# Performance work log

Measured on AMD Instinct MI355X. Metric: run time of the kernel, lower is better.

Reference implementation:

```python
import jax, jax.numpy as jnp
import numpy as np
from jax import lax

# ---- constants mirroring Prediction.__init__ kwargs ----
INP = 608
NUM_CLASSES = 20
ALPHA, BETA = 1.0, 0.5
OBJ_T, CONF_T, LOC_T = 0.6, 0.05, 0.5
NMS_T, SIZE_T, SIGMA = 0.1, 0.0, 0.5
TOP_K = 8
M_CAND = 256          # fixed-size candidate cap for jit-compatible NMS
NEG = -1e9            # sentinel for masked scores
ANCHORS = [[(116, 90), (156, 198), (373, 326)],
           [(30, 61), (62, 45), (59, 119)],
           [(10, 13), (16, 30), (33, 23)]]


def _decode(pred, anchors):
    """pred: (B, A, G, G, 6+C) raw level output -> decoded flat tensors."""
    B, A, G, _, C = pred.shape
    stride = INP // G
    xy = jax.nn.sigmoid(pred[..., 0:2])
    g = jnp.arange(G, dtype=pred.dtype)
    gx, gy = jnp.meshgrid(g, g)                      # gx[i,j]=j, gy[i,j]=i (np.meshgrid 'xy')
    off = jnp.stack([gx, gy], axis=-1)[None, None]   # (1,1,G,G,2)
    xy = ALPHA * xy - 0.5 * (ALPHA - 1.0) + off
    anc = jnp.asarray(anchors, dtype=pred.dtype) / stride  # (A,2) scaled to grid units
    wh = jnp.exp(pred[..., 2:4]) * anc[None, :, None, None, :]
    box = jnp.concatenate([xy, wh], axis=-1) * stride       # back to pixel units
    obj = jax.nn.sigmoid(pred[..., 4])
    loc = jax.nn.sigmoid(pred[..., 5])
    clsp = jax.nn.softmax(pred[..., 6:], axis=-1)
    N = A * G * G
    return (box.reshape(B, N, 4), obj.reshape(B, N),
            loc.reshape(B, N), clsp.reshape(B, N, NUM_CLASSES))


def _soft_nms(boxes, s0, cls):
    """Per-image Gaussian soft-NMS (class-aware), +1 pixel IoU convention as in bbox_iou.
    boxes: (M,4) xyxy, s0: (M,) scores (NEG for invalid), cls: (M,) int. Returns kept mask."""
    M = s0.shape[0]

    def step(carry, _):
        s, kept = carry
        j = jnp.argmax(s)
        do = s[j] >= NMS_T
        kept = kept | ((jnp.arange(M) == j) & do)
        bj = boxes[j]
        ix1 = jnp.maximum(bj[0], boxes[:, 0]); iy1 = jnp.maximum(bj[1], boxes[:, 1])
        ix2 = jnp.minimum(bj[2], boxes[:, 2]); iy2 = jnp.minimum(bj[3], boxes[:, 3])
        inter = jnp.maximum(ix2 - ix1 + 1.0, 0.0) * jnp.maximum(iy2 - iy1 + 1.0, 0.0)
        a1 = (bj[2] - bj[0] + 1.0) * (bj[3] - bj[1] + 1.0)
        a2 = (boxes[:, 2] - boxes[:, 0] + 1.0) * (boxes[:, 3] - boxes[:, 1] + 1.0)
        iou = inter / (a1 + a2 - inter + 1e-16)
        decay = jnp.exp(-(iou * iou) / SIGMA)
        s_new = jnp.where(cls == cls[j], s * decay, s).at[j].set(NEG)
        s = jnp.where(do, s_new, s)
        return (s, kept), None

    (_, kept), _ = lax.scan(step, (s0, jnp.zeros(M, dtype=bool)), None, length=M)
    return kept


def _forward(pred_l0, pred_l1, pred_l2):
    parts = [_decode(p, a) for p, a in zip([pred_l0, pred_l1, pred_l2], ANCHORS)]
    box = jnp.concatenate([p[0] for p in parts], axis=1)   # (B,N,4) xywh
    obj = jnp.concatenate([p[1] for p in parts], axis=1)
    loc = jnp.concatenate([p[2] for p in parts], axis=1)
    clsp = jnp.concatenate([p[3] for p in parts], axis=1)

    cx, cy, w, h = box[..., 0], box[..., 1], box[..., 2], box[..., 3]
    x1 = jnp.clip(cx - w / 2, 0.0, INP); y1 = jnp.clip(cy - h / 2, 0.0, INP)
    x2 = jnp.clip(cx + w / 2, 0.0, INP); y2 = jnp.clip(cy + h / 2, 0.0, INP)
    boxes = jnp.stack([x1, y1, x2, y2], axis=-1)            # (B,N,4) xyxy, clamped

    cls_conf = jnp.max(clsp, axis=-1)
    cls_id = jnp.argmax(clsp, axis=-1)
    area = (x2 - x1) * (y2 - y1)
    valid = ((obj >= OBJ_T) & (area >= INP * INP * SIZE_T)
             & (obj * cls_conf >= CONF_T) & (loc >= LOC_T))
    score = (obj * cls_conf) ** BETA * loc ** (1.0 - BETA)
    masked = jnp.where(valid, score, NEG)

    # fixed-size candidate set per image (descending-score sort + cap)
    vals, idx = lax.top_k(masked, M_CAND)                   # (B,M)
    cboxes = jnp.take_along_axis(boxes, idx[..., None], axis=1)
    ccls = jnp.take_along_axis(cls_id, idx, axis=1)
    s0 = jnp.where(vals > NEG / 2, vals, NEG)

    kept = jax.vmap(_soft_nms)(cboxes, s0, ccls)            # (B,M) bool

    # keep_top_k: top_k among kept, ranked by ORIGINAL (pre-decay) score
    fscore = jnp.where(kept, vals, NEG)
    fvals, fidx = lax.top_k(fscore, TOP_K)                  # (B,TOP_K)
    fboxes = jnp.take_along_axis(cboxes, fidx[..., None], axis=1)
    fcls = jnp.take_along_axis(ccls, fidx, axis=1)
    row = jnp.concatenate([fboxes, fvals[..., None],
                           fcls[..., None].astype(fboxes.dtype)], axis=-1)  # (B,K,6)
    ok = fvals > NEG / 2
    return jnp.where(ok[..., None], row, 0.0)


def setup_inputs() -> dict:
    key = jax.random.key(0)
    k0, k1, k2 = jax.random.split(key, 3)
    return {
        "pred_l0": jax.random.normal(k0, (64, 3, 19, 19, 26), dtype=jnp.float32),
        "pred_l1": jax.random.normal(k1, (64, 3, 38, 38, 26), dtype=jnp.float32),
        "pred_l2": jax.random.normal(k2, (64, 3, 76, 76, 26), dtype=jnp.float32),
    }


def reference(pred_l0, pred_l1, pred_l2):
    return _forward(pred_l0, pred_l1, pred_l2)
```

## Files before the change

kernel.cpp:

```cpp
#include <hip/hip_runtime.h>
#include <climits>

constexpr int kB  = 64;
constexpr int kG0 = 19, kG1 = 38, kG2 = 76;
constexpr int kN0 = 3 * kG0 * kG0;
constexpr int kN1 = 3 * kG1 * kG1;
constexpr int kN2 = 3 * kG2 * kG2;
constexpr int kN  = kN0 + kN1 + kN2;
constexpr int kM  = 256;
constexpr int kTopK = 8;
constexpr float kNEG = -1e9f;

constexpr int kT0 = 5, kT1 = 17, kT2 = 68;
constexpr int kTilesPerImg = kT0 + kT1 + kT2;
constexpr int kGridScore = 1920;
constexpr int kTilesPerBlk = 3;

__constant__ float c_anchors[3][3][2] = {
    {{116.f, 90.f}, {156.f, 198.f}, {373.f, 326.f}},
    {{30.f, 61.f},  {62.f, 45.f},   {59.f, 119.f}},
    {{10.f, 13.f},  {16.f, 30.f},   {33.f, 23.f}},
};

__device__ __forceinline__ float fexpf(float x) { return __expf(x); }
__device__ __forceinline__ float frcpf(float x) { return __builtin_amdgcn_rcpf(x); }
__device__ __forceinline__ float fsigm(float x) { return frcpf(1.0f + __expf(-x)); }

__device__ __forceinline__ unsigned score_to_key(float s) {
  unsigned fb = __float_as_uint(s);
  unsigned m = (fb & 0x80000000u) ? 0xFFFFFFFFu : 0x80000000u;
  return fb ^ m;
}
__device__ __forceinline__ float key_to_score(unsigned k) {
  unsigned fb = (k & 0x80000000u) ? (k ^ 0x80000000u) : ~k;
  return __uint_as_float(fb);
}

__device__ __forceinline__ const float* cell_ptr(
    const float* p0, const float* p1, const float* p2, int b, int n,
    int& lvl, int& a, int& gi, int& gj, float& stride) {
  const float* src; int G, m;
  if (n < kN0)            { src = p0; G = kG0; lvl = 0; m = n;             stride = 32.f; }
  else if (n < kN0 + kN1) { src = p1; G = kG1; lvl = 1; m = n - kN0;       stride = 16.f; }
  else                    { src = p2; G = kG2; lvl = 2; m = n - kN0 - kN1; stride = 8.f; }
  int gg = G * G;
  a = m / gg;
  int r = m - a * gg;
  gi = r / G;
  gj = r - gi * G;
  return src + (size_t)((((b * 3 + a) * G + gi) * G + gj)) * 26;
}

__device__ __forceinline__ void waveArgmax(float& v, int& i) {
  #pragma unroll
  for (int off = 1; off < 64; off <<= 1) {
    float ov = __shfl_xor(v, off);
    int oi = __shfl_xor(i, off);
    if (ov > v || (ov == v && oi < i)) { v = ov; i = oi; }
  }
}
__device__ __forceinline__ float waveMax(float v) {
  #pragma unroll
  for (int off = 1; off < 64; off <<= 1) v = fmaxf(v, __shfl_xor(v, off));
  return v;
}
__device__ __forceinline__ float sel4f(const float a[4], int q) {
  float r = a[0];
  r = (q == 1) ? a[1] : r;
  r = (q == 2) ? a[2] : r;
  r = (q == 3) ? a[3] : r;
  return r;
}
__device__ __forceinline__ int sel4i(const int a[4], int q) {
  int r = a[0];
  r = (q == 1) ? a[1] : r;
  r = (q == 2) ? a[2] : r;
  r = (q == 3) ? a[3] : r;
  return r;
}

__device__ __forceinline__ void async_copy16(const void* g, void* s) {
  __builtin_amdgcn_global_load_lds(
      (__attribute__((address_space(1))) unsigned int*)g,
      (__attribute__((address_space(3))) unsigned int*)s, 16, 0, 0);
}

__global__ void zero_kernel(int* __restrict__ cnt) {
  if ((int)threadIdx.x < kB) cnt[threadIdx.x] = 0;
}

__global__ __launch_bounds__(256) void score_kernel(
    const float* __restrict__ p0, const float* __restrict__ p1, const float* __restrict__ p2,
    unsigned long long* __restrict__ pairs, int* __restrict__ cnt)
{
  __shared__ float2 lds2[2][256 * 13];
  __shared__ int wTot[4];
  __shared__ int sBase;

  int t = threadIdx.x;
  int lane = t & 63, wave = t >> 6;

  const float* gb[kTilesPerBlk]; int nc[kTilesPerBlk], n0[kTilesPerBlk], bb[kTilesPerBlk];
  bool dmaOk[kTilesPerBlk];
  #pragma unroll
  for (int j = 0; j < kTilesPerBlk; ++j) {
    int tileId = (int)blockIdx.x + j * kGridScore;
    int b = tileId / kTilesPerImg;
    int r = tileId - b * kTilesPerImg;
    const float* slab; int NL, lvlOff, tile; bool lvl0 = false;
    if (r < kT0)            { slab = p0; NL = kN0; lvlOff = 0;         tile = r;            lvl0 = true; }
    else if (r < kT0 + kT1) { slab = p1; NL = kN1; lvlOff = kN0;       tile = r - kT0; }
    else                    { slab = p2; NL = kN2; lvlOff = kN0 + kN1; tile = r - kT0 - kT1; }
    int cellBase = tile * 256;
    nc[j] = min(256, NL - cellBase);
    gb[j] = slab + ((size_t)b * NL + cellBase) * 26;
    n0[j] = lvlOff + cellBase;
    bb[j] = b;
    dmaOk[j] = (!lvl0) && (nc[j] == 256);
  }

  auto stage = [&](int j, int buf) {
    if (dmaOk[j]) {
      const char* g = (const char*)gb[j];
      char* s = (char*)&lds2[buf][0];
      for (int c = wave; c < 26; c += 4)
        async_copy16(g + c * 1024 + lane * 16, s + c * 1024);
    } else {
      const float2* g2 = (const float2*)gb[j];
      float2* s2 = &lds2[buf][0];
      int tot = nc[j] * 13;
      for (int i = t; i < tot; i += 256) s2[i] = g2[i];
    }
  };

  stage(0, 0);
  #pragma unroll
  for (int j = 0; j < kTilesPerBlk; ++j) {
    __syncthreads();
    if (j + 1 < kTilesPerBlk) stage(j + 1, (j + 1) & 1);

    int curNc = nc[j], curN0 = n0[j], curB = bb[j];
    const float2* bufp = &lds2[j & 1][0];

    bool valid = false;
    unsigned long long pairVal = 0;
    if (t < curNc) {
      const float2* c2 = &bufp[t * 13];
      float2 ol = c2[2];
      float obj = fsigm(ol.x);
      float loc = fsigm(ol.y);
      float tch[20];
      #pragma unroll
      for (int q = 0; q < 10; ++q) { float2 v = c2[3 + q]; tch[2*q] = v.x; tch[2*q+1] = v.y; }
      float lm = tch[0];
      #pragma unroll
      for (int c = 1; c < 20; ++c) lm = fmaxf(lm, tch[c]);
      float se = 0.f;
      #pragma unroll
      for (int c = 0; c < 20; ++c) se += fexpf(tch[c] - lm);
      float cls_conf = frcpf(se);
      float conf = obj * cls_conf;
      if (obj >= 0.6f && loc >= 0.5f && conf >= 0.05f) {
        float score = sqrtf(conf) * sqrtf(loc);
        valid = true;
        pairVal = ((unsigned long long)score_to_key(score) << 32) | (unsigned)(curN0 + t);
      }
    }

    unsigned long long mask = __ballot(valid);
    int lanePfx = __popcll(mask & ((1ull << lane) - 1ull));
    if (lane == 0) wTot[wave] = __popcll(mask);
    __syncthreads();
    if (t == 0) {
      int tot = wTot[0] + wTot[1] + wTot[2] + wTot[3];
      sBase = (tot > 0) ? atomicAdd(&cnt[curB], tot) : 0;
    }
    __syncthreads();
    if (valid) {
      int waveOff = 0;
      #pragma unroll
      for (int q = 0; q < 4; ++q) if (q < wave) waveOff += wTot[q];
      pairs[(size_t)curB * kN + sBase + waveOff + lanePfx] = pairVal;
    }
  }
}

__device__ __forceinline__ void findThresholdBin(
    const int* hist, int NB, int needed,
    int& outB, int& outCumAbove, int& outTotal,
    int* shWave, int* shOut)
{
  int tid = threadIdx.x, lane = tid & 63, w = tid >> 6;
  if (tid == 0) { shOut[0] = -1; shOut[1] = 0; }
  int ipt = (NB + 511) / 512;
  int base = tid * ipt;
  int csum = 0;
  for (int i = 0; i < ipt; ++i) { int bn = base + i; if (bn < NB) csum += hist[bn]; }
  int v = csum;
  #pragma unroll
  for (int off = 1; off < 64; off <<= 1) {
    int tv = __shfl_down(v, off);
    if (lane + off < 64) v += tv;
  }
  if (lane == 0) shWave[w] = v;
  __syncthreads();
  int above = 0, total = 0;
  #pragma unroll
  for (int q = 0; q < 8; ++q) {
    int wt = shWave[q];
    total += wt;
    if (q > w) above += wt;
  }
  int S = v + above;
  if (S >= needed && S - csum < needed) {
    int running = S - csum;
    for (int i = ipt - 1; i >= 0; --i) {
      int bn = base + i; if (bn >= NB) continue;
      int c = hist[bn];
      if (running + c >= needed) { shOut[0] = bn; shOut[1] = running; break; }
      running += c;
    }
  }
  __syncthreads();
  outB = shOut[0]; outCumAbove = shOut[1]; outTotal = total;
  __syncthreads();
}

__global__ __launch_bounds__(512) void select_kernel(
    const unsigned long long* __restrict__ pairs, const int* __restrict__ cnt,
    int* __restrict__ candIdx, unsigned* __restrict__ candKey)
{
  int b = blockIdx.x, tid = threadIdx.x;
  const unsigned long long* kk = pairs + (size_t)b * kN;
  int NC = cnt[b];
  const unsigned keyNEG = score_to_key(kNEG);

  __shared__ int hist[4096];
  __shared__ int eqBuf[1024];
  __shared__ int shWave[8], shOut[2];
  __shared__ unsigned sT;
  __shared__ int sCgt;

  for (int i = tid; i < 4096; i += 512) hist[i] = 0;
  __syncthreads();
  for (int x = tid; x < NC; x += 512)
    atomicAdd(&hist[(unsigned)(kk[x] >> 52)], 1);
  __syncthreads();
  int B, cumAbove1, total1;
  findThresholdBin(hist, 4096, kM, B, cumAbove1, total1, shWave, shOut);

  if (total1 < kM) {
    if (tid == 0) { sT = keyNEG; sCgt = total1; }
    __syncthreads();
  } else {
    int needed2 = kM - cumAbove1;
    for (int i = tid; i < 4096; i += 512) hist[i] = 0;
    __syncthreads();
    for (int x = tid; x < NC; x += 512) {
      unsigned k = (unsigned)(kk[x] >> 32);
      if ((int)(k >> 20) == B) atomicAdd(&hist[(k >> 8) & 0xFFF], 1);
    }
    __syncthreads();
    int B2, cumAbove2, total2;
    findThresholdBin(hist, 4096, needed2, B2, cumAbove2, total2, shWave, shOut);
    int prefix24 = (B << 12) | B2;
    int needed3 = needed2 - cumAbove2;

    for (int i = tid; i < 256; i += 512) hist[i] = 0;
    __syncthreads();
    for (int x = tid; x < NC; x += 512) {
      unsigned k = (unsigned)(kk[x] >> 32);
      if ((int)(k >> 8) == prefix24) atomicAdd(&hist[k & 0xFF], 1);
    }
    __syncthreads();
    int B3, cumAbove3, total3;
    findThresholdBin(hist, 256, needed3, B3, cumAbove3, total3, shWave, shOut);
    if (tid == 0) {
      sT = ((unsigned)prefix24 << 8) | (unsigned)B3;
      sCgt = cumAbove1 + cumAbove2 + cumAbove3;
    }
    __syncthreads();
  }

  unsigned T = sT;
  int cgt = sCgt;

  __shared__ int sCnt, eqCnt;
  if (tid == 0) { sCnt = 0; eqCnt = 0; }
  __syncthreads();
  int* ci = candIdx + (size_t)b * kM;
  unsigned* ck = candKey + (size_t)b * kM;
  for (int x = tid; x < NC; x += 512) {
    unsigned long long v = kk[x];
    unsigned k = (unsigned)(v >> 32);
    if (k > T) {
      int p = atomicAdd(&sCnt, 1);
      ci[p] = (int)(unsigned)v; ck[p] = k;
    } else if (k == T && T != keyNEG) {
      int p = atomicAdd(&eqCnt, 1); if (p < 1024) eqBuf[p] = (int)(unsigned)v;
    }
  }
  __syncthreads();

  int needed = kM - cgt;
  if (T == keyNEG) {
    if (tid >= cgt && tid < kM) { ci[tid] = -1; ck[tid] = keyNEG; }
  } else {
    int ce = min(eqCnt, 1024);
    if (ce == needed) {
      if (tid < needed) { ci[cgt + tid] = eqBuf[tid]; ck[cgt + tid] = T; }
    } else if (tid == 0) {
      for (int q = 0; q < needed; ++q) {
        int mv = INT_MAX, mp = 0;
        for (int x = 0; x < ce; ++x) if (eqBuf[x] < mv) { mv = eqBuf[x]; mp = x; }
        ci[cgt + q] = mv; ck[cgt + q] = T; eqBuf[mp] = INT_MAX;
      }
    }
  }
}

__global__ __launch_bounds__(64) void nms_kernel(
    const float* __restrict__ p0, const float* __restrict__ p1, const float* __restrict__ p2,
    const int* __restrict__ candIdx, const unsigned* __restrict__ candKey,
    float* __restrict__ out)
{
  int b = blockIdx.x, lane = threadIdx.x;

  float x1[4], y1[4], x2[4], y2[4], val[4], s[4];
  int cls[4];
  bool kept[4];

  #pragma unroll
  for (int q = 0; q < 4; ++q) {
    int slot = b * kM + q * 64 + lane;
    int n = candIdx[slot];
    float sc = key_to_score(candKey[slot]);
    kept[q] = false;
    x1[q] = y1[q] = x2[q] = y2[q] = 0.f;
    cls[q] = 0; val[q] = sc; s[q] = sc;
    if (n >= 0) {
      int lvl, a, gi, gj; float stride;
      const float* p = cell_ptr(p0, p1, p2, b, n, lvl, a, gi, gj, stride);
      const float2* r2 = (const float2*)p;
      float2 c01 = r2[0], c23 = r2[1];
      float cx = (fsigm(c01.x) + (float)gj) * stride;
      float cy = (fsigm(c01.y) + (float)gi) * stride;
      float w = fexpf(c23.x) * c_anchors[lvl][a][0];
      float h = fexpf(c23.y) * c_anchors[lvl][a][1];
      x1[q] = fminf(fmaxf(cx - 0.5f * w, 0.f), 608.f);
      y1[q] = fminf(fmaxf(cy - 0.5f * h, 0.f), 608.f);
      x2[q] = fminf(fmaxf(cx + 0.5f * w, 0.f), 608.f);
      y2[q] = fminf(fmaxf(cy + 0.5f * h, 0.f), 608.f);
      float lm = -3.4e38f; int mc = 0;
      #pragma unroll
      for (int j = 3; j < 13; ++j) {
        float2 v = r2[j];
        int c0 = 2 * (j - 3);
        if (v.x > lm) { lm = v.x; mc = c0; }
        if (v.y > lm) { lm = v.y; mc = c0 + 1; }
      }
      cls[q] = mc;
    }
  }

  float top8[8];
  #pragma unroll
  for (int i = 0; i < 8; ++i) top8[i] = kNEG;
  int keptCount = 0;

  for (int it = 0; it < kM; ++it) {
    float bv = s[0]; int bq = 0;
    #pragma unroll
    for (int q = 1; q < 4; ++q) if (s[q] > bv) { bv = s[q]; bq = q; }
    int bi = bq * 64 + lane;
    waveArgmax(bv, bi);
    if (bv < 0.1f) break;

    int wlane = bi & 63, wq = bi >> 6;
    float jx1 = __shfl(sel4f(x1, wq), wlane);
    float jy1 = __shfl(sel4f(y1, wq), wlane);
    float jx2 = __shfl(sel4f(x2, wq), wlane);
    float jy2 = __shfl(sel4f(y2, wq), wlane);
    float jval = __shfl(sel4f(val, wq), wlane);
    int   cj  = __shfl(sel4i(cls, wq), wlane);

    float a1 = (jx2 - jx1 + 1.0f) * (jy2 - jy1 + 1.0f);
    #pragma unroll
    for (int q = 0; q < 4; ++q) {
      if (cls[q] == cj) {
        float ix1 = fmaxf(jx1, x1[q]), iy1 = fmaxf(jy1, y1[q]);
        float ix2 = fminf(jx2, x2[q]), iy2 = fminf(jy2, y2[q]);
        float inter = fmaxf(ix2 - ix1 + 1.0f, 0.0f) * fmaxf(iy2 - iy1 + 1.0f, 0.0f);
        float a2 = (x2[q] - x1[q] + 1.0f) * (y2[q] - y1[q] + 1.0f);
        float iou = inter / (a1 + a2 - inter + 1e-16f);
        s[q] *= fexpf(-(iou * iou) * 2.0f);
      }
      if (bi == q * 64 + lane) { kept[q] = true; s[q] = kNEG; }
    }

    float v = jval;
    #pragma unroll
    for (int i = 0; i < 8; ++i) { float m = fmaxf(top8[i], v); v = fminf(top8[i], v); top8[i] = m; }
    ++keptCount;
    if (keptCount >= kTopK) {
      float am = kNEG;
      #pragma unroll
      for (int q = 0; q < 4; ++q) if (s[q] >= 0.1f) am = fmaxf(am, val[q]);
      am = waveMax(am);
      if (am < top8[7]) break;
    }
  }

  float f[4];
  #pragma unroll
  for (int q = 0; q < 4; ++q) f[q] = kept[q] ? val[q] : kNEG;
  for (int k = 0; k < kTopK; ++k) {
    float bv = f[0]; int bq = 0;
    #pragma unroll
    for (int q = 1; q < 4; ++q) if (f[q] > bv) { bv = f[q]; bq = q; }
    int bi = bq * 64 + lane;
    waveArgmax(bv, bi);
    int wlane = bi & 63, wq = bi >> 6;
    if (lane == wlane) {
      float* o = out + (size_t)(b * kTopK + k) * 6;
      if (bv > kNEG * 0.5f) {
        o[0] = sel4f(x1, wq); o[1] = sel4f(y1, wq);
        o[2] = sel4f(x2, wq); o[3] = sel4f(y2, wq);
        o[4] = sel4f(val, wq); o[5] = (float)sel4i(cls, wq);
      } else {
        o[0] = 0.f; o[1] = 0.f; o[2] = 0.f; o[3] = 0.f; o[4] = 0.f; o[5] = 0.f;
      }
    }
    #pragma unroll
    for (int q = 0; q < 4; ++q) if (bi == q * 64 + lane) f[q] = kNEG;
  }
}

extern "C" void kernel_launch(void* const* d_in, const int* in_sizes, int n_in,
                              void* d_out, int out_size, void* d_ws, size_t ws_size,
                              hipStream_t stream) {
  const float* p0 = (const float*)d_in[0];
  const float* p1 = (const float*)d_in[1];
  const float* p2 = (const float*)d_in[2];
  float* out = (float*)d_out;

  unsigned long long* pairs = (unsigned long long*)d_ws;
  int* candIdx = (int*)(pairs + (size_t)kB * kN);
  unsigned* candKey = (unsigned*)(candIdx + kB * kM);
  int* cnt = (int*)(candKey + kB * kM);

  zero_kernel<<<1, 64, 0, stream>>>(cnt);
  score_kernel<<<kGridScore, 256, 0, stream>>>(p0, p1, p2, pairs, cnt);
  select_kernel<<<kB, 512, 0, stream>>>(pairs, cnt, candIdx, candKey);
  nms_kernel<<<kB, 64, 0, stream>>>(p0, p1, p2, candIdx, candKey, out);
}
```

Baseline: 243.3 us.

## Replace compacted key-index pairs with dense per-cell key array

```diff
diff --git a/kernel.cpp b/kernel.cpp
--- a/kernel.cpp
+++ b/kernel.cpp
@@ -85,17 +85,11 @@
       (__attribute__((address_space(3))) unsigned int*)s, 16, 0, 0);
 }
 
-__global__ void zero_kernel(int* __restrict__ cnt) {
-  if ((int)threadIdx.x < kB) cnt[threadIdx.x] = 0;
-}
-
 __global__ __launch_bounds__(256) void score_kernel(
     const float* __restrict__ p0, const float* __restrict__ p1, const float* __restrict__ p2,
-    unsigned long long* __restrict__ pairs, int* __restrict__ cnt)
+    unsigned* __restrict__ keys)
 {
   __shared__ float2 lds2[2][256 * 13];
-  __shared__ int wTot[4];
-  __shared__ int sBase;
 
   int t = threadIdx.x;
   int lane = t & 63, wave = t >> 6;
@@ -142,8 +136,6 @@
     int curNc = nc[j], curN0 = n0[j], curB = bb[j];
     const float2* bufp = &lds2[j & 1][0];
 
-    bool valid = false;
-    unsigned long long pairVal = 0;
     if (t < curNc) {
       const float2* c2 = &bufp[t * 13];
       float2 ol = c2[2];
@@ -160,27 +152,9 @@
       for (int c = 0; c < 20; ++c) se += fexpf(tch[c] - lm);
       float cls_conf = frcpf(se);
       float conf = obj * cls_conf;
-      if (obj >= 0.6f && loc >= 0.5f && conf >= 0.05f) {
-        float score = sqrtf(conf) * sqrtf(loc);
-        valid = true;
-        pairVal = ((unsigned long long)score_to_key(score) << 32) | (unsigned)(curN0 + t);
-      }
-    }
-
-    unsigned long long mask = __ballot(valid);
-    int lanePfx = __popcll(mask & ((1ull << lane) - 1ull));
-    if (lane == 0) wTot[wave] = __popcll(mask);
-    __syncthreads();
-    if (t == 0) {
-      int tot = wTot[0] + wTot[1] + wTot[2] + wTot[3];
-      sBase = (tot > 0) ? atomicAdd(&cnt[curB], tot) : 0;
-    }
-    __syncthreads();
-    if (valid) {
-      int waveOff = 0;
-      #pragma unroll
-      for (int q = 0; q < 4; ++q) if (q < wave) waveOff += wTot[q];
-      pairs[(size_t)curB * kN + sBase + waveOff + lanePfx] = pairVal;
+      float masked = (obj >= 0.6f && loc >= 0.5f && conf >= 0.05f)
+                     ? sqrtf(conf) * sqrtf(loc) : kNEG;
+      keys[(size_t)curB * kN + curN0 + t] = score_to_key(masked);
     }
   }
 }
@@ -227,12 +201,10 @@
 }
 
 __global__ __launch_bounds__(512) void select_kernel(
-    const unsigned long long* __restrict__ pairs, const int* __restrict__ cnt,
-    int* __restrict__ candIdx, unsigned* __restrict__ candKey)
+    const unsigned* __restrict__ keys, int* __restrict__ candIdx, unsigned* __restrict__ candKey)
 {
   int b = blockIdx.x, tid = threadIdx.x;
-  const unsigned long long* kk = pairs + (size_t)b * kN;
-  int NC = cnt[b];
+  const unsigned* kk = keys + (size_t)b * kN;
   const unsigned keyNEG = score_to_key(kNEG);
 
   __shared__ int hist[4096];
@@ -243,8 +215,10 @@
 
   for (int i = tid; i < 4096; i += 512) hist[i] = 0;
   __syncthreads();
-  for (int x = tid; x < NC; x += 512)
-    atomicAdd(&hist[(unsigned)(kk[x] >> 52)], 1);
+  for (int x = tid; x < kN; x += 512) {
+    unsigned k = kk[x];
+    if (k >= 0x80000000u) atomicAdd(&hist[k >> 20], 1);
+  }
   __syncthreads();
   int B, cumAbove1, total1;
   findThresholdBin(hist, 4096, kM, B, cumAbove1, total1, shWave, shOut);
@@ -256,8 +230,8 @@
     int needed2 = kM - cumAbove1;
     for (int i = tid; i < 4096; i += 512) hist[i] = 0;
     __syncthreads();
-    for (int x = tid; x < NC; x += 512) {
-      unsigned k = (unsigned)(kk[x] >> 32);
+    for (int x = tid; x < kN; x += 512) {
+      unsigned k = kk[x];
       if ((int)(k >> 20) == B) atomicAdd(&hist[(k >> 8) & 0xFFF], 1);
     }
     __syncthreads();
@@ -268,8 +242,8 @@
 
     for (int i = tid; i < 256; i += 512) hist[i] = 0;
     __syncthreads();
-    for (int x = tid; x < NC; x += 512) {
-      unsigned k = (unsigned)(kk[x] >> 32);
+    for (int x = tid; x < kN; x += 512) {
+      unsigned k = kk[x];
       if ((int)(k >> 8) == prefix24) atomicAdd(&hist[k & 0xFF], 1);
     }
     __syncthreads();
@@ -290,14 +264,13 @@
   __syncthreads();
   int* ci = candIdx + (size_t)b * kM;
   unsigned* ck = candKey + (size_t)b * kM;
-  for (int x = tid; x < NC; x += 512) {
-    unsigned long long v = kk[x];
-    unsigned k = (unsigned)(v >> 32);
+  for (int x = tid; x < kN; x += 512) {
+    unsigned k = kk[x];
     if (k > T) {
       int p = atomicAdd(&sCnt, 1);
-      ci[p] = (int)(unsigned)v; ck[p] = k;
+      ci[p] = x; ck[p] = k;
     } else if (k == T && T != keyNEG) {
-      int p = atomicAdd(&eqCnt, 1); if (p < 1024) eqBuf[p] = (int)(unsigned)v;
+      int p = atomicAdd(&eqCnt, 1); if (p < 1024) eqBuf[p] = x;
     }
   }
   __syncthreads();
@@ -444,13 +417,11 @@
   const float* p2 = (const float*)d_in[2];
   float* out = (float*)d_out;
 
-  unsigned long long* pairs = (unsigned long long*)d_ws;
-  int* candIdx = (int*)(pairs + (size_t)kB * kN);
+  unsigned* keys = (unsigned*)d_ws;
+  int* candIdx = (int*)(keys + (size_t)kB * kN);
   unsigned* candKey = (unsigned*)(candIdx + kB * kM);
-  int* cnt = (int*)(candKey + kB * kM);
-
-  zero_kernel<<<1, 64, 0, stream>>>(cnt);
-  score_kernel<<<kGridScore, 256, 0, stream>>>(p0, p1, p2, pairs, cnt);
-  select_kernel<<<kB, 512, 0, stream>>>(pairs, cnt, candIdx, candKey);
+
+  score_kernel<<<kGridScore, 256, 0, stream>>>(p0, p1, p2, keys);
+  select_kernel<<<kB, 512, 0, stream>>>(keys, candIdx, candKey);
   nms_kernel<<<kB, 64, 0, stream>>>(p0, p1, p2, candIdx, candKey, out);
 }
```

Result: slower. 265.4 us (+9.1%).
